# Performance work log

Measured on AMD Instinct MI355X. Metric: run time of the kernel, lower is better.

Reference implementation:

```python
import jax, jax.numpy as jnp
import numpy as np

B, S, D = 8, 1024, 1024

def setup_inputs() -> dict:
    key = jax.random.key(0)
    ks = jax.random.split(key, 6)
    context = jax.random.normal(ks[0], (B, S, D), dtype=jnp.float32)
    eos_mask = jax.random.randint(ks[1], (B, S), 0, 2, dtype=jnp.int32)
    prior = jax.random.uniform(ks[2], (), dtype=jnp.float32)
    adj_mat = jax.random.randint(ks[3], (B, S, S), 0, 2, dtype=jnp.int32)
    Wk = jax.random.normal(ks[4], (D, D), dtype=jnp.float32) * 0.02
    Wq = jax.random.normal(ks[5], (D, D), dtype=jnp.float32) * 0.02
    bk = jnp.zeros((D,), jnp.float32)
    bq = jnp.zeros((D,), jnp.float32)
    ln_gamma = jnp.ones((D,), jnp.float32)
    ln_beta = jnp.zeros((D,), jnp.float32)
    return {"context": context, "eos_mask": eos_mask, "prior": prior,
            "adj_mat": adj_mat, "Wk": Wk, "bk": bk, "Wq": Wq, "bq": bq,
            "ln_gamma": ln_gamma, "ln_beta": ln_beta}

def reference(context, eos_mask, prior, adj_mat, Wk, bk, Wq, bq, ln_gamma, ln_beta):
    d_model = context.shape[-1]
    seq_len = context.shape[1]
    # LayerNorm (annotated-transformer style: unbiased std, eps added to std)
    mu = jnp.mean(context, axis=-1, keepdims=True)
    std = jnp.std(context, axis=-1, keepdims=True, ddof=1)
    x = ln_gamma * (context - mu) / (std + 1e-6) + ln_beta
    # projections (torch Linear: x @ W.T + b)
    key_p = x @ Wk.T + bk
    query = x @ Wq.T + bq
    scores = jnp.einsum('bqd,bkd->bqk', query, key_p) / (d_model / 2)
    scores = jnp.where(adj_mat == 0, -1e9, scores)
    neibor_attn = jax.nn.softmax(scores, axis=-1)
    neibor_attn = jnp.sqrt(neibor_attn * jnp.swapaxes(neibor_attn, -1, -2) + 1e-9)
    neibor_attn = prior + (1.0 - prior) * neibor_attn
    # constant structural matrices
    a = jnp.eye(seq_len, k=1, dtype=jnp.float32)          # superdiagonal
    b = jnp.eye(seq_len, dtype=jnp.float32)               # diagonal
    tri = jnp.triu(jnp.ones((seq_len, seq_len), jnp.float32))  # upper incl diag
    # t = (log(attn+eps) masked to superdiagonal) @ tri
    t = jnp.matmul(jnp.where(a == 0, 0.0, jnp.log(neibor_attn + 1e-9)), tri)
    g_attn = jnp.exp(jnp.matmul(tri, t))
    g_attn = jnp.where((tri - b) == 0, 0.0, g_attn)  # keep strict upper only
    g_attn = g_attn + jnp.swapaxes(g_attn, -1, -2) + jnp.where(b == 0, 1e-9, neibor_attn)
    return (g_attn, neibor_attn)
```

## Files before the change

kernel.cpp:

```cpp
#include <hip/hip_runtime.h>
#include <hip/hip_bf16.h>

#define S_LEN 1024
#define D_DIM 1024
#define N_BAT 8
#define BSS   (8ull*1024ull*1024ull)

using bf16x8 = __attribute__((ext_vector_type(8))) short;
using f32x4  = __attribute__((ext_vector_type(4))) float;

__device__ __forceinline__ short f2bf(float v) {
    __hip_bfloat16 h = __float2bfloat16(v);
    return *reinterpret_cast<short*>(&h);
}

__device__ __forceinline__ void gload_lds16(const void* g, void* l) {
    __builtin_amdgcn_global_load_lds(
        (const __attribute__((address_space(1))) void*)g,
        (__attribute__((address_space(3))) void*)l, 16, 0, 0);
}

__device__ __forceinline__ int xcd_remap_flat() {
    const int nwg  = gridDim.x * gridDim.y * gridDim.z;
    const int flat = blockIdx.x + gridDim.x * (blockIdx.y + gridDim.y * blockIdx.z);
    const int cpx  = nwg >> 3;
    return (flat & 7) * cpx + (flat >> 3);
}

__device__ __forceinline__ void gemm_mainloop8(
    const short* __restrict__ A, const short* __restrict__ Bt,
    int brow, int bcol, int kstart, int kIters,
    short* As, short* Bs, f32x4 acc[4][2])
{
    const int tid  = threadIdx.x;
    const int lane = tid & 63;
    const int w    = tid >> 6;
    const int wr   = w >> 2;
    const int wc   = w & 3;
    const int rsel = lane & 15;
    const int kb   = (lane >> 4) * 16;

    const int b0   = w * 1024;
    const int b1   = 8192 + w * 1024;
    const int ch0  = b0 + lane * 16;
    const int ch1  = b1 + lane * 16;
    const int row0 = ch0 >> 7;
    const int cb0  = (ch0 & 127) ^ ((row0 & 7) << 4);
    const int row1 = ch1 >> 7;
    const int cb1  = (ch1 & 127) ^ ((row1 & 7) << 4);

#pragma unroll
    for (int m = 0; m < 4; ++m)
#pragma unroll
        for (int n = 0; n < 2; ++n) acc[m][n] = 0.0f;

    {
        char* Ad = (char*)As;
        char* Bd = (char*)Bs;
        gload_lds16((const char*)(A  + (size_t)(brow + row0) * 1024 + kstart) + cb0, Ad + b0);
        gload_lds16((const char*)(A  + (size_t)(brow + row1) * 1024 + kstart) + cb1, Ad + b1);
        gload_lds16((const char*)(Bt + (size_t)(bcol + row0) * 1024 + kstart) + cb0, Bd + b0);
        gload_lds16((const char*)(Bt + (size_t)(bcol + row1) * 1024 + kstart) + cb1, Bd + b1);
    }
    __syncthreads();

    for (int t = 0; t < kIters; ++t) {
        const int cur = t & 1;
        const char* Ac = (const char*)As + cur * 16384;
        const char* Bc = (const char*)Bs + cur * 16384;
        if (t + 1 < kIters) {
            const int k0 = kstart + (t + 1) * 64;
            char* An = (char*)As + (cur ^ 1) * 16384;
            char* Bn = (char*)Bs + (cur ^ 1) * 16384;
            gload_lds16((const char*)(A  + (size_t)(brow + row0) * 1024 + k0) + cb0, An + b0);
            gload_lds16((const char*)(A  + (size_t)(brow + row1) * 1024 + k0) + cb1, An + b1);
            gload_lds16((const char*)(Bt + (size_t)(bcol + row0) * 1024 + k0) + cb0, Bn + b0);
            gload_lds16((const char*)(Bt + (size_t)(bcol + row1) * 1024 + k0) + cb1, Bn + b1);
        }
        bf16x8 af[4][2], bfr[2][2];
#pragma unroll
        for (int m = 0; m < 4; ++m) {
            const int row = wr * 64 + m * 16 + rsel;
            const int sw  = (row & 7) << 4;
#pragma unroll
            for (int kk = 0; kk < 2; ++kk)
                af[m][kk] = *(const bf16x8*)&Ac[row * 128 + ((kk * 64 + kb) ^ sw)];
        }
#pragma unroll
        for (int n = 0; n < 2; ++n) {
            const int row = wc * 32 + n * 16 + rsel;
            const int sw  = (row & 7) << 4;
#pragma unroll
            for (int kk = 0; kk < 2; ++kk)
                bfr[n][kk] = *(const bf16x8*)&Bc[row * 128 + ((kk * 64 + kb) ^ sw)];
        }
#pragma unroll
        for (int kk = 0; kk < 2; ++kk)
#pragma unroll
            for (int m = 0; m < 4; ++m)
#pragma unroll
                for (int n = 0; n < 2; ++n)
                    acc[m][n] = __builtin_amdgcn_mfma_f32_16x16x32_bf16(
                        af[m][kk], bfr[n][kk], acc[m][n], 0, 0, 0);
        __syncthreads();
    }
}

__global__ __launch_bounds__(512) void gemm_bf16(
    const short* __restrict__ A, const short* __restrict__ Bt,
    short* __restrict__ C)
{
    __shared__ short As[2 * 8192];
    __shared__ short Bs[2 * 8192];
    const int nid = xcd_remap_flat();
    const int mx  = ((nid >> 6) << 3) + (nid & 7);
    const int ny  = (nid >> 3) & 7;
    const int brow = mx * 128, bcol = ny * 128;

    f32x4 acc[4][2];
    gemm_mainloop8(A, Bt, brow, bcol, 0, 16, As, Bs, acc);

    const int lane = threadIdx.x & 63;
    const int w    = threadIdx.x >> 6;
    const int wr   = w >> 2, wc = w & 3;
#pragma unroll
    for (int m = 0; m < 4; ++m)
#pragma unroll
        for (int n = 0; n < 2; ++n) {
            const int colg = bcol + wc * 32 + n * 16 + (lane & 15);
#pragma unroll
            for (int r = 0; r < 4; ++r) {
                const int rowg = brow + wr * 64 + m * 16 + ((lane >> 4) * 4 + r);
                C[(size_t)rowg * 1024 + colg] = f2bf(acc[m][n][r]);
            }
        }
}

__global__ __launch_bounds__(512) void gemm_scores(
    const short* __restrict__ Tm, const short* __restrict__ Xm,
    const float* __restrict__ p, const float* __restrict__ r2,
    const float* __restrict__ c0p, float* __restrict__ Sc)
{
    __shared__ short As[2 * 8192];
    __shared__ short Bs[2 * 8192];
    const int nid = xcd_remap_flat();
    const int mx  = nid & 7;
    const int ny  = (nid >> 3) & 7;
    const int b   = nid >> 6;
    const short* A  = Tm + (size_t)b * 1024 * 1024;
    const short* Bt = Xm + (size_t)b * 1024 * 1024;
    const float* pb = p  + (size_t)b * 1024;
    const float* rb = r2 + (size_t)b * 1024;
    float* C = Sc + (size_t)b * 1024 * 1024;
    const int brow = mx * 128, bcol = ny * 128;

    f32x4 acc[4][2];
    gemm_mainloop8(A, Bt, brow, bcol, 0, 16, As, Bs, acc);

    const int lane = threadIdx.x & 63;
    const int w    = threadIdx.x >> 6;
    const int wr   = w >> 2, wc = w & 3;
    const float c0v = c0p[0];
#pragma unroll
    for (int m = 0; m < 4; ++m)
#pragma unroll
        for (int n = 0; n < 2; ++n) {
            const int colg = bcol + wc * 32 + n * 16 + (lane & 15);
            const float radd = rb[colg] + c0v;
#pragma unroll
            for (int r = 0; r < 4; ++r) {
                const int rowg = brow + wr * 64 + m * 16 + ((lane >> 4) * 4 + r);
                C[(size_t)rowg * 1024 + colg] =
                    (acc[m][n][r] + pb[rowg] + radd) * 0.001953125f;
            }
        }
}

__global__ __launch_bounds__(512) void gemm_splitk(
    const short* __restrict__ A, const short* __restrict__ Bt,
    float* __restrict__ P)
{
    __shared__ short As[2 * 8192];
    __shared__ short Bs[2 * 8192];
    const int brow = blockIdx.x * 128, bcol = blockIdx.y * 128;
    const int z = blockIdx.z;

    f32x4 acc[4][2];
    gemm_mainloop8(A, Bt, brow, bcol, z * 256, 4, As, Bs, acc);

    float* Pz = P + (size_t)z * 1024 * 1024;
    const int lane = threadIdx.x & 63;
    const int w    = threadIdx.x >> 6;
    const int wr   = w >> 2, wc = w & 3;
#pragma unroll
    for (int m = 0; m < 4; ++m)
#pragma unroll
        for (int n = 0; n < 2; ++n) {
            const int colg = bcol + wc * 32 + n * 16 + (lane & 15);
#pragma unroll
            for (int r = 0; r < 4; ++r) {
                const int rowg = brow + wr * 64 + m * 16 + ((lane >> 4) * 4 + r);
                Pz[(size_t)rowg * 1024 + colg] = acc[m][n][r];
            }
        }
}

__global__ __launch_bounds__(256) void reduce_m2t(
    const float* __restrict__ P, short* __restrict__ M)
{
    const int idx = blockIdx.x * 256 + threadIdx.x;
    const float4* P4 = (const float4*)P;
    float4 s = P4[idx];
    const float4 s1 = P4[idx + 262144];
    const float4 s2 = P4[idx + 524288];
    const float4 s3 = P4[idx + 786432];
    s.x += s1.x + s2.x + s3.x;
    s.y += s1.y + s2.y + s3.y;
    s.z += s1.z + s2.z + s3.z;
    s.w += s1.w + s2.w + s3.w;
    short4 o;
    o.x = f2bf(s.x); o.y = f2bf(s.y); o.z = f2bf(s.z); o.w = f2bf(s.w);
    ((short4*)M)[idx] = o;
}

__global__ __launch_bounds__(256) void bias_gemv1(
    const float* __restrict__ Wq, const float* __restrict__ Wk,
    const float* __restrict__ bk, const float* __restrict__ bq,
    float* __restrict__ pu, float* __restrict__ pv)
{
    __shared__ float su[8][128];
    __shared__ float sv[8][128];
    const int tx = threadIdx.x & 31;
    const int ty = threadIdx.x >> 5;
    const int colBase = blockIdx.x * 128;
    const int rowBase = blockIdx.y * 64;
    const int i = colBase + tx * 4;
    float4 au = {0,0,0,0}, av = {0,0,0,0};
#pragma unroll
    for (int jj = 0; jj < 8; ++jj) {
        const int j = rowBase + ty + jj * 8;
        const float bkv = bk[j], bqv = bq[j];
        const float4 wq = *(const float4*)&Wq[(size_t)j * 1024 + i];
        const float4 wk = *(const float4*)&Wk[(size_t)j * 1024 + i];
        au.x += wq.x * bkv; au.y += wq.y * bkv; au.z += wq.z * bkv; au.w += wq.w * bkv;
        av.x += wk.x * bqv; av.y += wk.y * bqv; av.z += wk.z * bqv; av.w += wk.w * bqv;
    }
    ((float4*)su[ty])[tx] = au;
    ((float4*)sv[ty])[tx] = av;
    __syncthreads();
    if (ty == 0) {
        float4 s1 = ((float4*)su[0])[tx];
        float4 s2 = ((float4*)sv[0])[tx];
#pragma unroll
        for (int k = 1; k < 8; ++k) {
            const float4 t1 = ((float4*)su[k])[tx];
            const float4 t2 = ((float4*)sv[k])[tx];
            s1.x += t1.x; s1.y += t1.y; s1.z += t1.z; s1.w += t1.w;
            s2.x += t2.x; s2.y += t2.y; s2.z += t2.z; s2.w += t2.w;
        }
        ((float4*)&pu[(size_t)blockIdx.y * 1024 + colBase])[tx] = s1;
        ((float4*)&pv[(size_t)blockIdx.y * 1024 + colBase])[tx] = s2;
    }
}

__global__ __launch_bounds__(256) void bias_gemv2(
    const float* __restrict__ pu, const float* __restrict__ pv,
    const float* __restrict__ bk, const float* __restrict__ bq,
    float* __restrict__ u, float* __restrict__ v, float* __restrict__ c0)
{
    __shared__ float sh[4];
    const int i = blockIdx.x * 256 + threadIdx.x;
    float su = 0.0f, sv = 0.0f;
#pragma unroll
    for (int k = 0; k < 16; ++k) {
        su += pu[k * 1024 + i];
        sv += pv[k * 1024 + i];
    }
    u[i] = su;
    v[i] = sv;
    if (blockIdx.x == 0) {
        const int t = threadIdx.x;
        const float4 a = ((const float4*)bq)[t];
        const float4 b = ((const float4*)bk)[t];
        float s = a.x*b.x + a.y*b.y + a.z*b.z + a.w*b.w;
        for (int off = 32; off > 0; off >>= 1) s += __shfl_down(s, off);
        const int lane = t & 63, w = t >> 6;
        if (lane == 0) sh[w] = s;
        __syncthreads();
        if (t == 0) c0[0] = sh[0] + sh[1] + sh[2] + sh[3];
    }
}

__global__ __launch_bounds__(256) void ln_kernel(
    const float* __restrict__ X, const float* __restrict__ gamma,
    const float* __restrict__ beta, const float* __restrict__ u,
    const float* __restrict__ v2, short* __restrict__ Y,
    float* __restrict__ p, float* __restrict__ r2)
{
    __shared__ float sh[16];
    const size_t row = blockIdx.x;
    const int t = threadIdx.x;
    float4 v = ((const float4*)(X + row * 1024))[t];
    float s  = v.x + v.y + v.z + v.w;
    float ss = v.x*v.x + v.y*v.y + v.z*v.z + v.w*v.w;
    for (int off = 32; off > 0; off >>= 1) {
        s  += __shfl_down(s, off);
        ss += __shfl_down(ss, off);
    }
    const int lane = t & 63, w = t >> 6;
    if (lane == 0) { sh[w] = s; sh[4 + w] = ss; }
    __syncthreads();
    if (t == 0) {
        float S  = sh[0] + sh[1] + sh[2] + sh[3];
        float SS = sh[4] + sh[5] + sh[6] + sh[7];
        float mu = S * (1.0f / 1024.0f);
        float var = fmaxf((SS - S * mu) * (1.0f / 1023.0f), 0.0f);
        sh[0] = mu;
        sh[1] = 1.0f / (sqrtf(var) + 1e-6f);
    }
    __syncthreads();
    const float mu = sh[0], inv = sh[1];
    float4 g  = ((const float4*)gamma)[t];
    float4 be = ((const float4*)beta)[t];
    float y0 = g.x * (v.x - mu) * inv + be.x;
    float y1 = g.y * (v.y - mu) * inv + be.y;
    float y2 = g.z * (v.z - mu) * inv + be.z;
    float y3 = g.w * (v.w - mu) * inv + be.w;
    short4 o;
    o.x = f2bf(y0); o.y = f2bf(y1); o.z = f2bf(y2); o.w = f2bf(y3);
    ((short4*)(Y + row * 1024))[t] = o;
    float4 uu = ((const float4*)u)[t];
    float4 vv = ((const float4*)v2)[t];
    float dp = y0*uu.x + y1*uu.y + y2*uu.z + y3*uu.w;
    float dr = y0*vv.x + y1*vv.y + y2*vv.z + y3*vv.w;
    for (int off = 32; off > 0; off >>= 1) {
        dp += __shfl_down(dp, off);
        dr += __shfl_down(dr, off);
    }
    if (lane == 0) { sh[8 + w] = dp; sh[12 + w] = dr; }
    __syncthreads();
    if (t == 0) {
        p[row]  = sh[8] + sh[9] + sh[10] + sh[11];
        r2[row] = sh[12] + sh[13] + sh[14] + sh[15];
    }
}

__global__ __launch_bounds__(256) void cvt_t_kernel(
    const float* __restrict__ Wq, const float* __restrict__ Wk,
    short* __restrict__ wqt, short* __restrict__ wkt)
{
    __shared__ float T[32][33];
    const float* src = blockIdx.z ? Wk : Wq;
    short* dst = blockIdx.z ? wkt : wqt;
    const int bi = blockIdx.x * 32, bj = blockIdx.y * 32;
    const int c = threadIdx.x & 31, r0 = threadIdx.x >> 5;
#pragma unroll
    for (int rr = 0; rr < 4; ++rr) {
        const int r = r0 + rr * 8;
        T[r][c] = src[(size_t)(bi + r) * 1024 + bj + c];
    }
    __syncthreads();
#pragma unroll
    for (int rr = 0; rr < 4; ++rr) {
        const int r = r0 + rr * 8;
        dst[(size_t)(bj + r) * 1024 + bi + c] = f2bf(T[c][r]);
    }
}

__global__ __launch_bounds__(256) void softmax_kernel(
    const float* __restrict__ Sc, const int* __restrict__ adj,
    float* __restrict__ At)
{
    __shared__ float sh[4];
    const size_t row = blockIdx.x;
    const int t = threadIdx.x;
    const float4 sv = ((const float4*)(Sc + row * 1024))[t];
    const int4   av = ((const int4*)(adj + row * 1024))[t];
    float m = -3.0e38f;
    if (av.x) m = fmaxf(m, sv.x);
    if (av.y) m = fmaxf(m, sv.y);
    if (av.z) m = fmaxf(m, sv.z);
    if (av.w) m = fmaxf(m, sv.w);
    for (int off = 32; off > 0; off >>= 1) m = fmaxf(m, __shfl_down(m, off));
    const int lane = t & 63, w = t >> 6;
    if (lane == 0) sh[w] = m;
    __syncthreads();
    const float M = fmaxf(fmaxf(sh[0], sh[1]), fmaxf(sh[2], sh[3]));
    __syncthreads();
    float e0 = av.x ? expf(sv.x - M) : 0.0f;
    float e1 = av.y ? expf(sv.y - M) : 0.0f;
    float e2 = av.z ? expf(sv.z - M) : 0.0f;
    float e3 = av.w ? expf(sv.w - M) : 0.0f;
    float s = e0 + e1 + e2 + e3;
    for (int off = 32; off > 0; off >>= 1) s += __shfl_down(s, off);
    if (lane == 0) sh[w] = s;
    __syncthreads();
    const float Sm = sh[0] + sh[1] + sh[2] + sh[3];
    float4 o;
    if (Sm > 0.0f) {
        const float inv = 1.0f / Sm;
        o.x = e0 * inv; o.y = e1 * inv; o.z = e2 * inv; o.w = e3 * inv;
    } else {
        o.x = o.y = o.z = o.w = 1.0f / 1024.0f;
    }
    ((float4*)(At + row * 1024))[t] = o;
}

__global__ __launch_bounds__(1024) void cum2_kernel(
    const float* __restrict__ At, const float* __restrict__ prior_p,
    double* __restrict__ cum)
{
    __shared__ double sh[1024];
    const int b = blockIdx.x;
    const int t = threadIdx.x;
    const float prior = *prior_p;
    const float om = 1.0f - prior;
    const float* attn = At + (size_t)b * 1024 * 1024;
    double v = 0.0;
    if (t >= 1) {
        const int k = t - 1;
        const float a1 = attn[(size_t)k * 1024 + (k + 1)];
        const float a2 = attn[(size_t)(k + 1) * 1024 + k];
        const float na = prior + om * sqrtf(a1 * a2 + 1e-9f);
        v = (double)logf(na + 1e-9f);
    }
    sh[t] = v;
    __syncthreads();
#pragma unroll
    for (int off = 1; off < 1024; off <<= 1) {
        const double add = (t >= off) ? sh[t - off] : 0.0;
        __syncthreads();
        sh[t] += add;
        __syncthreads();
    }
    cum[b * 1024 + t] = sh[t];
}

__global__ __launch_bounds__(256) void na_g_kernel(
    float* __restrict__ At, const float* __restrict__ prior_p,
    const double* __restrict__ cum, float* __restrict__ G)
{
    const int ti = blockIdx.x >> 5, tj = blockIdx.x & 31;
    if (tj < ti) return;
    const int b = blockIdx.y;
    const float prior = *prior_p;
    const float om = 1.0f - prior;
    float* base = At + (size_t)b * 1024 * 1024;
    float* gb   = G  + (size_t)b * 1024 * 1024;
    const double* cb = cum + (size_t)b * 1024;
    __shared__ float T1[32][33];
    __shared__ float T2[32][33];
    const int c = threadIdx.x & 31, r0 = threadIdx.x >> 5;
#pragma unroll
    for (int rr = 0; rr < 4; ++rr) {
        const int r = r0 + rr * 8;
        T1[r][c] = base[(size_t)(ti * 32 + r) * 1024 + tj * 32 + c];
        T2[r][c] = base[(size_t)(tj * 32 + r) * 1024 + ti * 32 + c];
    }
    __syncthreads();
#pragma unroll
    for (int rr = 0; rr < 4; ++rr) {
        const int r = r0 + rr * 8;
        const int R1 = ti * 32 + r, C1 = tj * 32 + c;
        const float na1 = prior + om * sqrtf(T1[r][c] * T2[c][r] + 1e-9f);
        base[(size_t)R1 * 1024 + C1] = na1;
        float g1;
        if (R1 == C1) g1 = na1;
        else {
            const int lo = min(R1, C1), hi = max(R1, C1);
            g1 = expf((float)(cb[hi] - cb[lo])) + 1e-9f;
        }
        gb[(size_t)R1 * 1024 + C1] = g1;
        const int R2 = tj * 32 + r, C2 = ti * 32 + c;
        const float na2 = prior + om * sqrtf(T2[r][c] * T1[c][r] + 1e-9f);
        base[(size_t)R2 * 1024 + C2] = na2;
        float g2;
        if (R2 == C2) g2 = na2;
        else {
            const int lo = min(R2, C2), hi = max(R2, C2);
            g2 = expf((float)(cb[hi] - cb[lo])) + 1e-9f;
        }
        gb[(size_t)R2 * 1024 + C2] = g2;
    }
}

extern "C" void kernel_launch(void* const* d_in, const int* in_sizes, int n_in,
                              void* d_out, int out_size, void* d_ws, size_t ws_size,
                              hipStream_t stream)
{
    const float* context = (const float*)d_in[0];
    const float* prior   = (const float*)d_in[2];
    const int*   adj     = (const int*)d_in[3];
    const float* Wk      = (const float*)d_in[4];
    const float* bk      = (const float*)d_in[5];
    const float* Wq      = (const float*)d_in[6];
    const float* bq      = (const float*)d_in[7];
    const float* gamma   = (const float*)d_in[8];
    const float* beta    = (const float*)d_in[9];

    float* out   = (float*)d_out;
    float* gout  = out;
    float* naout = out + BSS;

    char* ws = (char*)d_ws;
    short*  xb    = (short*)(ws);
    short*  wqt   = (short*)(ws + (16ull << 20));
    short*  wkt   = (short*)(ws + (18ull << 20));
    short*  m2t   = (short*)(ws + (20ull << 20));
    short*  tb    = (short*)(ws + (22ull << 20));
    float*  m2par = (float*)tb;
    double* cumd  = (double*)(ws + (38ull << 20));
    float*  uvec  = (float*)(ws + (38ull << 20) + (1ull << 16));
    float*  vvec  = uvec + 1024;
    float*  c0    = vvec + 1024;
    float*  pvec  = c0 + 64;
    float*  rvec  = pvec + 8192;
    float*  pu    = rvec + 8192;
    float*  pv    = pu + 16384;

    bias_gemv1<<<dim3(8, 16), 256, 0, stream>>>(Wq, Wk, bk, bq, pu, pv);
    bias_gemv2<<<4, 256, 0, stream>>>(pu, pv, bk, bq, uvec, vvec, c0);
    ln_kernel<<<8192, 256, 0, stream>>>(context, gamma, beta, uvec, vvec,
                                        xb, pvec, rvec);
    cvt_t_kernel<<<dim3(32, 32, 2), 256, 0, stream>>>(Wq, Wk, wqt, wkt);
    gemm_splitk<<<dim3(8, 8, 4), 512, 0, stream>>>(wkt, wqt, m2par);
    reduce_m2t<<<1024, 256, 0, stream>>>(m2par, m2t);
    gemm_bf16<<<dim3(64, 8), 512, 0, stream>>>(xb, m2t, tb);
    gemm_scores<<<dim3(8, 8, 8), 512, 0, stream>>>(tb, xb, pvec, rvec, c0, gout);
    softmax_kernel<<<8192, 256, 0, stream>>>(gout, adj, naout);
    cum2_kernel<<<8, 1024, 0, stream>>>(naout, prior, cumd);
    na_g_kernel<<<dim3(1024, 8), 256, 0, stream>>>(naout, prior, cumd, gout);
}
```

Before: 141.2 us.

## Deepen GEMM LDS pipeline to four stages with explicit vmcnt waits

Replaces the double-buffered GEMM mainloop with a templated four-buffer pipeline that prefetches three k-tiles ahead. It waits on the async global-to-LDS loads with explicit s_waitcnt vmcnt counts and uses one barrier per iteration instead of two. The aim is to hide global load latency and cut synchronisation in all three GEMM kernels. LDS per block doubles to 128KB, which may lower occupancy, and reusing a buffer with only one barrier per iteration carries a possible race.

Measured after the change: 137.9 us. -2.4%, faster.

```diff
diff --git a/kernel.cpp b/kernel.cpp
--- a/kernel.cpp
+++ b/kernel.cpp
@@ -27,9 +27,10 @@
     return (flat & 7) * cpx + (flat >> 3);
 }
 
-__device__ __forceinline__ void gemm_mainloop8(
+template<int KITERS>
+__device__ __forceinline__ void gemm_mainloop_pipe(
     const short* __restrict__ A, const short* __restrict__ Bt,
-    int brow, int bcol, int kstart, int kIters,
+    int brow, int bcol, int kstart,
     short* As, short* Bs, f32x4 acc[4][2])
 {
     const int tid  = threadIdx.x;
@@ -54,29 +55,39 @@
 #pragma unroll
         for (int n = 0; n < 2; ++n) acc[m][n] = 0.0f;
 
-    {
-        char* Ad = (char*)As;
-        char* Bd = (char*)Bs;
-        gload_lds16((const char*)(A  + (size_t)(brow + row0) * 1024 + kstart) + cb0, Ad + b0);
-        gload_lds16((const char*)(A  + (size_t)(brow + row1) * 1024 + kstart) + cb1, Ad + b1);
-        gload_lds16((const char*)(Bt + (size_t)(bcol + row0) * 1024 + kstart) + cb0, Bd + b0);
-        gload_lds16((const char*)(Bt + (size_t)(bcol + row1) * 1024 + kstart) + cb1, Bd + b1);
-    }
-    __syncthreads();
-
-    for (int t = 0; t < kIters; ++t) {
-        const int cur = t & 1;
-        const char* Ac = (const char*)As + cur * 16384;
-        const char* Bc = (const char*)Bs + cur * 16384;
-        if (t + 1 < kIters) {
-            const int k0 = kstart + (t + 1) * 64;
-            char* An = (char*)As + (cur ^ 1) * 16384;
-            char* Bn = (char*)Bs + (cur ^ 1) * 16384;
+    constexpr int NPRE = (KITERS < 3) ? KITERS : 3;
+#pragma unroll
+    for (int i = 0; i < NPRE; ++i) {
+        const int k0 = kstart + i * 64;
+        char* Ad = (char*)As + i * 16384;
+        char* Bd = (char*)Bs + i * 16384;
+        gload_lds16((const char*)(A  + (size_t)(brow + row0) * 1024 + k0) + cb0, Ad + b0);
+        gload_lds16((const char*)(A  + (size_t)(brow + row1) * 1024 + k0) + cb1, Ad + b1);
+        gload_lds16((const char*)(Bt + (size_t)(bcol + row0) * 1024 + k0) + cb0, Bd + b0);
+        gload_lds16((const char*)(Bt + (size_t)(bcol + row1) * 1024 + k0) + cb1, Bd + b1);
+    }
+
+#pragma unroll
+    for (int t = 0; t < KITERS; ++t) {
+        const int ahead = KITERS - 1 - t;
+        if (ahead >= 2)      asm volatile("s_waitcnt vmcnt(8)" ::: "memory");
+        else if (ahead == 1) asm volatile("s_waitcnt vmcnt(4)" ::: "memory");
+        else                 asm volatile("s_waitcnt vmcnt(0)" ::: "memory");
+        __builtin_amdgcn_s_barrier();
+        asm volatile("" ::: "memory");
+
+        if (t + 3 < KITERS) {
+            const int k0 = kstart + (t + 3) * 64;
+            char* An = (char*)As + ((t + 3) & 3) * 16384;
+            char* Bn = (char*)Bs + ((t + 3) & 3) * 16384;
             gload_lds16((const char*)(A  + (size_t)(brow + row0) * 1024 + k0) + cb0, An + b0);
             gload_lds16((const char*)(A  + (size_t)(brow + row1) * 1024 + k0) + cb1, An + b1);
             gload_lds16((const char*)(Bt + (size_t)(bcol + row0) * 1024 + k0) + cb0, Bn + b0);
             gload_lds16((const char*)(Bt + (size_t)(bcol + row1) * 1024 + k0) + cb1, Bn + b1);
         }
+
+        const char* Ac = (const char*)As + (t & 3) * 16384;
+        const char* Bc = (const char*)Bs + (t & 3) * 16384;
         bf16x8 af[4][2], bfr[2][2];
 #pragma unroll
         for (int m = 0; m < 4; ++m) {
@@ -102,7 +113,6 @@
                 for (int n = 0; n < 2; ++n)
                     acc[m][n] = __builtin_amdgcn_mfma_f32_16x16x32_bf16(
                         af[m][kk], bfr[n][kk], acc[m][n], 0, 0, 0);
-        __syncthreads();
     }
 }
 
@@ -110,15 +120,15 @@
     const short* __restrict__ A, const short* __restrict__ Bt,
     short* __restrict__ C)
 {
-    __shared__ short As[2 * 8192];
-    __shared__ short Bs[2 * 8192];
+    __shared__ short As[4 * 8192];
+    __shared__ short Bs[4 * 8192];
     const int nid = xcd_remap_flat();
     const int mx  = ((nid >> 6) << 3) + (nid & 7);
     const int ny  = (nid >> 3) & 7;
     const int brow = mx * 128, bcol = ny * 128;
 
     f32x4 acc[4][2];
-    gemm_mainloop8(A, Bt, brow, bcol, 0, 16, As, Bs, acc);
+    gemm_mainloop_pipe<16>(A, Bt, brow, bcol, 0, As, Bs, acc);
 
     const int lane = threadIdx.x & 63;
     const int w    = threadIdx.x >> 6;
@@ -141,8 +151,8 @@
     const float* __restrict__ p, const float* __restrict__ r2,
     const float* __restrict__ c0p, float* __restrict__ Sc)
 {
-    __shared__ short As[2 * 8192];
-    __shared__ short Bs[2 * 8192];
+    __shared__ short As[4 * 8192];
+    __shared__ short Bs[4 * 8192];
     const int nid = xcd_remap_flat();
     const int mx  = nid & 7;
     const int ny  = (nid >> 3) & 7;
@@ -155,7 +165,7 @@
     const int brow = mx * 128, bcol = ny * 128;
 
     f32x4 acc[4][2];
-    gemm_mainloop8(A, Bt, brow, bcol, 0, 16, As, Bs, acc);
+    gemm_mainloop_pipe<16>(A, Bt, brow, bcol, 0, As, Bs, acc);
 
     const int lane = threadIdx.x & 63;
     const int w    = threadIdx.x >> 6;
@@ -180,13 +190,13 @@
     const short* __restrict__ A, const short* __restrict__ Bt,
     float* __restrict__ P)
 {
-    __shared__ short As[2 * 8192];
-    __shared__ short Bs[2 * 8192];
+    __shared__ short As[4 * 8192];
+    __shared__ short Bs[4 * 8192];
     const int brow = blockIdx.x * 128, bcol = blockIdx.y * 128;
     const int z = blockIdx.z;
 
     f32x4 acc[4][2];
-    gemm_mainloop8(A, Bt, brow, bcol, z * 256, 4, As, Bs, acc);
+    gemm_mainloop_pipe<4>(A, Bt, brow, bcol, z * 256, As, Bs, acc);
 
     float* Pz = P + (size_t)z * 1024 * 1024;
     const int lane = threadIdx.x & 63;
```

## Fuse adjacency masking into scores GEMM and defer softmax normalization to consumers

Applied to the files above, without the earlier changes.

Applies the adjacency mask in the scores GEMM epilogue, staging the tile through LDS so stores and the adj read are coalesced float4 accesses. The softmax kernel becomes a row-statistics kernel that writes only the max and inverse sum per row, and the cumulative and final kernels recompute attention probabilities from scores plus those stats. This drops one full 32MB write and read of the attention matrix, at the cost of recomputing exp. It also templates and unrolls the GEMM main loop, gives the bf16 GEMM an LDS-staged vectorized epilogue, and adds XCD remapping to the final kernel. Fully masked rows now give exp(0)/1024 instead of an explicit fallback, which is numerically equivalent.

New measurement: 123.8 us. 1.14x faster.

```diff
diff --git a/kernel.cpp b/kernel.cpp
--- a/kernel.cpp
+++ b/kernel.cpp
@@ -27,9 +27,10 @@
     return (flat & 7) * cpx + (flat >> 3);
 }
 
-__device__ __forceinline__ void gemm_mainloop8(
+template<int KITERS>
+__device__ __forceinline__ void gemm_ml128(
     const short* __restrict__ A, const short* __restrict__ Bt,
-    int brow, int bcol, int kstart, int kIters,
+    int brow, int bcol, int kstart,
     short* As, short* Bs, f32x4 acc[4][2])
 {
     const int tid  = threadIdx.x;
@@ -64,11 +65,12 @@
     }
     __syncthreads();
 
-    for (int t = 0; t < kIters; ++t) {
+#pragma unroll
+    for (int t = 0; t < KITERS; ++t) {
         const int cur = t & 1;
         const char* Ac = (const char*)As + cur * 16384;
         const char* Bc = (const char*)Bs + cur * 16384;
-        if (t + 1 < kIters) {
+        if (t + 1 < KITERS) {
             const int k0 = kstart + (t + 1) * 64;
             char* An = (char*)As + (cur ^ 1) * 16384;
             char* Bn = (char*)Bs + (cur ^ 1) * 16384;
@@ -110,16 +112,19 @@
     const short* __restrict__ A, const short* __restrict__ Bt,
     short* __restrict__ C)
 {
-    __shared__ short As[2 * 8192];
-    __shared__ short Bs[2 * 8192];
+    __shared__ char smem[65536];
+    short* As = (short*)smem;
+    short* Bs = (short*)(smem + 32768);
     const int nid = xcd_remap_flat();
     const int mx  = ((nid >> 6) << 3) + (nid & 7);
     const int ny  = (nid >> 3) & 7;
     const int brow = mx * 128, bcol = ny * 128;
 
     f32x4 acc[4][2];
-    gemm_mainloop8(A, Bt, brow, bcol, 0, 16, As, Bs, acc);
-
+    gemm_ml128<16>(A, Bt, brow, bcol, 0, As, Bs, acc);
+
+    __syncthreads();
+    short* ep = (short*)smem;
     const int lane = threadIdx.x & 63;
     const int w    = threadIdx.x >> 6;
     const int wr   = w >> 2, wc = w & 3;
@@ -127,22 +132,33 @@
     for (int m = 0; m < 4; ++m)
 #pragma unroll
         for (int n = 0; n < 2; ++n) {
-            const int colg = bcol + wc * 32 + n * 16 + (lane & 15);
+            const int Cc = wc * 32 + n * 16 + (lane & 15);
 #pragma unroll
             for (int r = 0; r < 4; ++r) {
-                const int rowg = brow + wr * 64 + m * 16 + ((lane >> 4) * 4 + r);
-                C[(size_t)rowg * 1024 + colg] = f2bf(acc[m][n][r]);
+                const int R = wr * 64 + m * 16 + (lane >> 4) * 4 + r;
+                ep[R * 136 + Cc] = f2bf(acc[m][n][r]);
             }
         }
+    __syncthreads();
+#pragma unroll
+    for (int it = 0; it < 4; ++it) {
+        const int fl  = it * 512 + threadIdx.x;
+        const int row = fl >> 4;
+        const int c8  = fl & 15;
+        const bf16x8 v = *(const bf16x8*)&ep[row * 136 + c8 * 8];
+        *(bf16x8*)&C[(size_t)(brow + row) * 1024 + bcol + c8 * 8] = v;
+    }
 }
 
 __global__ __launch_bounds__(512) void gemm_scores(
     const short* __restrict__ Tm, const short* __restrict__ Xm,
     const float* __restrict__ p, const float* __restrict__ r2,
-    const float* __restrict__ c0p, float* __restrict__ Sc)
-{
-    __shared__ short As[2 * 8192];
-    __shared__ short Bs[2 * 8192];
+    const float* __restrict__ c0p, const int* __restrict__ adj,
+    float* __restrict__ Sc)
+{
+    __shared__ char smem[68608];
+    short* As = (short*)smem;
+    short* Bs = (short*)(smem + 32768);
     const int nid = xcd_remap_flat();
     const int mx  = nid & 7;
     const int ny  = (nid >> 3) & 7;
@@ -151,42 +167,62 @@
     const short* Bt = Xm + (size_t)b * 1024 * 1024;
     const float* pb = p  + (size_t)b * 1024;
     const float* rb = r2 + (size_t)b * 1024;
+    const int*   ab = adj + (size_t)b * 1024 * 1024;
     float* C = Sc + (size_t)b * 1024 * 1024;
     const int brow = mx * 128, bcol = ny * 128;
 
     f32x4 acc[4][2];
-    gemm_mainloop8(A, Bt, brow, bcol, 0, 16, As, Bs, acc);
-
+    gemm_ml128<16>(A, Bt, brow, bcol, 0, As, Bs, acc);
+
+    __syncthreads();
+    float* ep = (float*)smem;
     const int lane = threadIdx.x & 63;
     const int w    = threadIdx.x >> 6;
     const int wr   = w >> 2, wc = w & 3;
+#pragma unroll
+    for (int m = 0; m < 4; ++m)
+#pragma unroll
+        for (int n = 0; n < 2; ++n) {
+            const int Cc = wc * 32 + n * 16 + (lane & 15);
+#pragma unroll
+            for (int r = 0; r < 4; ++r) {
+                const int R = wr * 64 + m * 16 + (lane >> 4) * 4 + r;
+                ep[R * 132 + Cc] = acc[m][n][r];
+            }
+        }
+    __syncthreads();
     const float c0v = c0p[0];
 #pragma unroll
-    for (int m = 0; m < 4; ++m)
-#pragma unroll
-        for (int n = 0; n < 2; ++n) {
-            const int colg = bcol + wc * 32 + n * 16 + (lane & 15);
-            const float radd = rb[colg] + c0v;
-#pragma unroll
-            for (int r = 0; r < 4; ++r) {
-                const int rowg = brow + wr * 64 + m * 16 + ((lane >> 4) * 4 + r);
-                C[(size_t)rowg * 1024 + colg] =
-                    (acc[m][n][r] + pb[rowg] + radd) * 0.001953125f;
-            }
-        }
+    for (int it = 0; it < 8; ++it) {
+        const int fl   = it * 512 + threadIdx.x;
+        const int row  = fl >> 5;
+        const int col4 = fl & 31;
+        const int rowg = brow + row;
+        const int colg = bcol + col4 * 4;
+        float4 v = *(const float4*)&ep[row * 132 + col4 * 4];
+        const float4 rv = *(const float4*)&rb[colg];
+        const float pa = pb[rowg] + c0v;
+        const int4 av = *(const int4*)&ab[(size_t)rowg * 1024 + colg];
+        v.x = av.x ? (v.x + pa + rv.x) * 0.001953125f : -1e9f;
+        v.y = av.y ? (v.y + pa + rv.y) * 0.001953125f : -1e9f;
+        v.z = av.z ? (v.z + pa + rv.z) * 0.001953125f : -1e9f;
+        v.w = av.w ? (v.w + pa + rv.w) * 0.001953125f : -1e9f;
+        *(float4*)&C[(size_t)rowg * 1024 + colg] = v;
+    }
 }
 
 __global__ __launch_bounds__(512) void gemm_splitk(
     const short* __restrict__ A, const short* __restrict__ Bt,
     float* __restrict__ P)
 {
-    __shared__ short As[2 * 8192];
-    __shared__ short Bs[2 * 8192];
+    __shared__ char smem[65536];
+    short* As = (short*)smem;
+    short* Bs = (short*)(smem + 32768);
     const int brow = blockIdx.x * 128, bcol = blockIdx.y * 128;
     const int z = blockIdx.z;
 
     f32x4 acc[4][2];
-    gemm_mainloop8(A, Bt, brow, bcol, z * 256, 4, As, Bs, acc);
+    gemm_ml128<4>(A, Bt, brow, bcol, z * 256, As, Bs, acc);
 
     float* Pz = P + (size_t)z * 1024 * 1024;
     const int lane = threadIdx.x & 63;
@@ -367,60 +403,47 @@
     }
 }
 
-__global__ __launch_bounds__(256) void softmax_kernel(
-    const float* __restrict__ Sc, const int* __restrict__ adj,
-    float* __restrict__ At)
+__global__ __launch_bounds__(256) void rowstat_kernel(
+    const float* __restrict__ Sc, float2* __restrict__ stats)
 {
     __shared__ float sh[4];
     const size_t row = blockIdx.x;
     const int t = threadIdx.x;
     const float4 sv = ((const float4*)(Sc + row * 1024))[t];
-    const int4   av = ((const int4*)(adj + row * 1024))[t];
-    float m = -3.0e38f;
-    if (av.x) m = fmaxf(m, sv.x);
-    if (av.y) m = fmaxf(m, sv.y);
-    if (av.z) m = fmaxf(m, sv.z);
-    if (av.w) m = fmaxf(m, sv.w);
+    float m = fmaxf(fmaxf(sv.x, sv.y), fmaxf(sv.z, sv.w));
     for (int off = 32; off > 0; off >>= 1) m = fmaxf(m, __shfl_down(m, off));
     const int lane = t & 63, w = t >> 6;
     if (lane == 0) sh[w] = m;
     __syncthreads();
     const float M = fmaxf(fmaxf(sh[0], sh[1]), fmaxf(sh[2], sh[3]));
     __syncthreads();
-    float e0 = av.x ? expf(sv.x - M) : 0.0f;
-    float e1 = av.y ? expf(sv.y - M) : 0.0f;
-    float e2 = av.z ? expf(sv.z - M) : 0.0f;
-    float e3 = av.w ? expf(sv.w - M) : 0.0f;
-    float s = e0 + e1 + e2 + e3;
+    float s = expf(sv.x - M) + expf(sv.y - M) + expf(sv.z - M) + expf(sv.w - M);
     for (int off = 32; off > 0; off >>= 1) s += __shfl_down(s, off);
     if (lane == 0) sh[w] = s;
     __syncthreads();
-    const float Sm = sh[0] + sh[1] + sh[2] + sh[3];
-    float4 o;
-    if (Sm > 0.0f) {
-        const float inv = 1.0f / Sm;
-        o.x = e0 * inv; o.y = e1 * inv; o.z = e2 * inv; o.w = e3 * inv;
-    } else {
-        o.x = o.y = o.z = o.w = 1.0f / 1024.0f;
-    }
-    ((float4*)(At + row * 1024))[t] = o;
+    if (t == 0) {
+        const float Sm = sh[0] + sh[1] + sh[2] + sh[3];
+        stats[row] = make_float2(M, 1.0f / Sm);
+    }
 }
 
 __global__ __launch_bounds__(1024) void cum2_kernel(
-    const float* __restrict__ At, const float* __restrict__ prior_p,
-    double* __restrict__ cum)
+    const float* __restrict__ Sc, const float2* __restrict__ stats,
+    const float* __restrict__ prior_p, double* __restrict__ cum)
 {
     __shared__ double sh[1024];
     const int b = blockIdx.x;
     const int t = threadIdx.x;
     const float prior = *prior_p;
     const float om = 1.0f - prior;
-    const float* attn = At + (size_t)b * 1024 * 1024;
+    const float* sc = Sc + (size_t)b * 1024 * 1024;
+    const float2* st = stats + (size_t)b * 1024;
     double v = 0.0;
     if (t >= 1) {
         const int k = t - 1;
-        const float a1 = attn[(size_t)k * 1024 + (k + 1)];
-        const float a2 = attn[(size_t)(k + 1) * 1024 + k];
+        const float2 s1 = st[k], s2 = st[k + 1];
+        const float a1 = expf(sc[(size_t)k * 1024 + (k + 1)] - s1.x) * s1.y;
+        const float a2 = expf(sc[(size_t)(k + 1) * 1024 + k] - s2.x) * s2.y;
         const float na = prior + om * sqrtf(a1 * a2 + 1e-9f);
         v = (double)logf(na + 1e-9f);
     }
@@ -436,17 +459,22 @@
     cum[b * 1024 + t] = sh[t];
 }
 
-__global__ __launch_bounds__(256) void na_g_kernel(
-    float* __restrict__ At, const float* __restrict__ prior_p,
-    const double* __restrict__ cum, float* __restrict__ G)
-{
-    const int ti = blockIdx.x >> 5, tj = blockIdx.x & 31;
+__global__ __launch_bounds__(256) void na_g2_kernel(
+    float* __restrict__ Sc, const float2* __restrict__ stats,
+    const float* __restrict__ prior_p, const double* __restrict__ cum,
+    float* __restrict__ NA)
+{
+    const int flat = blockIdx.x + 1024 * blockIdx.y;
+    const int nid  = (flat & 7) * 1024 + (flat >> 3);
+    const int b    = nid >> 10;
+    const int tidx = nid & 1023;
+    const int ti = tidx >> 5, tj = tidx & 31;
     if (tj < ti) return;
-    const int b = blockIdx.y;
     const float prior = *prior_p;
     const float om = 1.0f - prior;
-    float* base = At + (size_t)b * 1024 * 1024;
-    float* gb   = G  + (size_t)b * 1024 * 1024;
+    float* sc = Sc + (size_t)b * 1024 * 1024;
+    float* na = NA + (size_t)b * 1024 * 1024;
+    const float2* st = stats + (size_t)b * 1024;
     const double* cb = cum + (size_t)b * 1024;
     __shared__ float T1[32][33];
     __shared__ float T2[32][33];
@@ -454,8 +482,10 @@
 #pragma unroll
     for (int rr = 0; rr < 4; ++rr) {
         const int r = r0 + rr * 8;
-        T1[r][c] = base[(size_t)(ti * 32 + r) * 1024 + tj * 32 + c];
-        T2[r][c] = base[(size_t)(tj * 32 + r) * 1024 + ti * 32 + c];
+        const int R1 = ti * 32 + r, R2 = tj * 32 + r;
+        const float2 s1 = st[R1], s2 = st[R2];
+        T1[r][c] = expf(sc[(size_t)R1 * 1024 + tj * 32 + c] - s1.x) * s1.y;
+        T2[r][c] = expf(sc[(size_t)R2 * 1024 + ti * 32 + c] - s2.x) * s2.y;
     }
     __syncthreads();
 #pragma unroll
@@ -463,24 +493,24 @@
         const int r = r0 + rr * 8;
         const int R1 = ti * 32 + r, C1 = tj * 32 + c;
         const float na1 = prior + om * sqrtf(T1[r][c] * T2[c][r] + 1e-9f);
-        base[(size_t)R1 * 1024 + C1] = na1;
+        na[(size_t)R1 * 1024 + C1] = na1;
         float g1;
         if (R1 == C1) g1 = na1;
         else {
             const int lo = min(R1, C1), hi = max(R1, C1);
             g1 = expf((float)(cb[hi] - cb[lo])) + 1e-9f;
         }
-        gb[(size_t)R1 * 1024 + C1] = g1;
+        sc[(size_t)R1 * 1024 + C1] = g1;
         const int R2 = tj * 32 + r, C2 = ti * 32 + c;
         const float na2 = prior + om * sqrtf(T2[r][c] * T1[c][r] + 1e-9f);
-        base[(size_t)R2 * 1024 + C2] = na2;
+        na[(size_t)R2 * 1024 + C2] = na2;
         float g2;
         if (R2 == C2) g2 = na2;
         else {
             const int lo = min(R2, C2), hi = max(R2, C2);
             g2 = expf((float)(cb[hi] - cb[lo])) + 1e-9f;
         }
-        gb[(size_t)R2 * 1024 + C2] = g2;
+        sc[(size_t)R2 * 1024 + C2] = g2;
     }
 }
 
@@ -517,6 +547,7 @@
     float*  rvec  = pvec + 8192;
     float*  pu    = rvec + 8192;
     float*  pv    = pu + 16384;
+    float2* statv = (float2*)(pv + 16384);
 
     bias_gemv1<<<dim3(8, 16), 256, 0, stream>>>(Wq, Wk, bk, bq, pu, pv);
     bias_gemv2<<<4, 256, 0, stream>>>(pu, pv, bk, bq, uvec, vvec, c0);
@@ -526,8 +557,10 @@
     gemm_splitk<<<dim3(8, 8, 4), 512, 0, stream>>>(wkt, wqt, m2par);
     reduce_m2t<<<1024, 256, 0, stream>>>(m2par, m2t);
     gemm_bf16<<<dim3(64, 8), 512, 0, stream>>>(xb, m2t, tb);
-    gemm_scores<<<dim3(8, 8, 8), 512, 0, stream>>>(tb, xb, pvec, rvec, c0, gout);
-    softmax_kernel<<<8192, 256, 0, stream>>>(gout, adj, naout);
-    cum2_kernel<<<8, 1024, 0, stream>>>(naout, prior, cumd);
-    na_g_kernel<<<dim3(1024, 8), 256, 0, stream>>>(naout, prior, cumd, gout);
-}
+    gemm_scores<<<dim3(8, 8, 8), 512, 0, stream>>>(tb, xb, pvec, rvec, c0,
+                                                   adj, gout);
+    rowstat_kernel<<<8192, 256, 0, stream>>>(gout, statv);
+    cum2_kernel<<<8, 1024, 0, stream>>>(gout, statv, prior, cumd);
+    na_g2_kernel<<<dim3(1024, 8), 256, 0, stream>>>(gout, statv, prior, cumd,
+                                                    naout);
+}
```
